# Kernel optimization log

Hardware: AMD Instinct MI355X
Metric: run time of the kernel (lower is better)

Reference implementation:

```python
import jax, jax.numpy as jnp
import numpy as np

EPS = 1e-08
CCE_WEIGHT = 1.0
DICE_WEIGHT = 0.5


def setup_inputs() -> dict:
    key = jax.random.key(0)
    k1, k2 = jax.random.split(key)
    B, C = 4194304, 8
    predictions = jax.random.normal(k1, (B, C), dtype=jnp.float32)
    labels = jax.random.randint(k2, (B,), 0, C)
    ground_truth = jax.nn.one_hot(labels, C, dtype=jnp.float32)  # one-hot, in [0,1]
    class_weights = jnp.array([1.0, 2.0, 1.5, 0.5, 1.0, 3.0, 0.75, 1.25], dtype=jnp.float32)
    return {"predictions": predictions, "ground_truth": ground_truth, "class_weights": class_weights}


def reference(predictions, ground_truth, class_weights):
    C = class_weights.shape[0]
    p = jax.nn.softmax(predictions, axis=1)            # [B, C]
    pred_cat = jnp.argmax(p, axis=1)                   # [B]
    gt_cat = jnp.argmax(ground_truth, axis=1)          # [B]

    # Confusion matrix: single fused scatter-add (replaces per-sample torch loop)
    cm = jnp.zeros((C, C), dtype=p.dtype).at[gt_cat, pred_cat].add(1.0)
    tp = jnp.diagonal(cm)
    fp = cm.sum(axis=0) - tp
    fn = cm.sum(axis=1) - tp
    dice = (tp + EPS) / (tp + fp + fn + EPS)
    dice_loss = jnp.mean((1.0 - dice) * class_weights)

    # Faithful to the original: cross_entropy is applied to the *softmaxed*
    # predictions (double softmax), with soft (probability) targets and
    # per-class weights; reduction='mean' over the batch.
    log_p2 = jax.nn.log_softmax(p, axis=1)             # log_softmax(softmax(x))
    ce_per_sample = -jnp.sum(class_weights * ground_truth * log_p2, axis=1)  # [B]
    cce_loss = jnp.mean(ce_per_sample)

    return cce_loss * CCE_WEIGHT + dice_loss * DICE_WEIGHT
```

## Files before the change

### kernel.cpp

```cpp
#include <hip/hip_runtime.h>


#define NBLOCKS 2048
#define NTHREADS 256

__device__ __forceinline__ float fast_exp(float x) { return __expf(x); }

__global__ void wcd_init(unsigned int* __restrict__ cnt) {
    int i = threadIdx.x;
    if (i < 24) cnt[i] = 0u;
}

__global__ __launch_bounds__(NTHREADS) void wcd_main(
    const float* __restrict__ pred, const float* __restrict__ gt,
    const float* __restrict__ cw, unsigned int* __restrict__ cnt,
    float* __restrict__ ce_partial, int B)
{
    __shared__ float sw[8];
    __shared__ unsigned int scnt[24];
    __shared__ float sred[NTHREADS];

    const int tid = threadIdx.x;
    if (tid < 8)  sw[tid]   = cw[tid];
    if (tid < 24) scnt[tid] = 0u;
    __syncthreads();

    float ce = 0.0f;
    const int stride = gridDim.x * blockDim.x;
    for (int i = blockIdx.x * blockDim.x + tid; i < B; i += stride) {
        const float4* p4 = reinterpret_cast<const float4*>(pred) + 2 * (size_t)i;
        const float4* g4 = reinterpret_cast<const float4*>(gt)   + 2 * (size_t)i;
        float4 a0 = p4[0], a1 = p4[1];
        float4 b0 = g4[0], b1 = g4[1];
        float x[8] = {a0.x, a0.y, a0.z, a0.w, a1.x, a1.y, a1.z, a1.w};
        float g[8] = {b0.x, b0.y, b0.z, b0.w, b1.x, b1.y, b1.z, b1.w};

        float m = x[0]; int am = 0;
        #pragma unroll
        for (int j = 1; j < 8; ++j) { if (x[j] > m) { m = x[j]; am = j; } }

        int gi = 0;
        #pragma unroll
        for (int j = 1; j < 8; ++j) { if (g[j] > 0.5f) gi = j; }

        float e[8], se = 0.0f;
        #pragma unroll
        for (int j = 0; j < 8; ++j) { e[j] = fast_exp(x[j] - m); se += e[j]; }
        float inv = 1.0f / se;

        float s2 = 0.0f, pg = 0.0f;
        #pragma unroll
        for (int j = 0; j < 8; ++j) {
            float pj = e[j] * inv;
            s2 += fast_exp(pj);
            if (j == gi) pg = pj;
        }
        ce += sw[gi] * (__logf(s2) - pg);

        atomicAdd(&scnt[gi], 1u);
        atomicAdd(&scnt[8 + am], 1u);
        if (gi == am) atomicAdd(&scnt[16 + gi], 1u);
    }

    sred[tid] = ce;
    __syncthreads();
    #pragma unroll
    for (int s = NTHREADS / 2; s > 0; s >>= 1) {
        if (tid < s) sred[tid] += sred[tid + s];
        __syncthreads();
    }
    if (tid == 0) ce_partial[blockIdx.x] = sred[0];

    if (tid < 24 && scnt[tid] != 0u) atomicAdd(&cnt[tid], scnt[tid]);
}

__global__ __launch_bounds__(NTHREADS) void wcd_finalize(
    const unsigned int* __restrict__ cnt, const float* __restrict__ ce_partial,
    const float* __restrict__ cw, float* __restrict__ out, int B)
{
    __shared__ float sred[NTHREADS];
    const int tid = threadIdx.x;
    float s = 0.0f;
    for (int i = tid; i < NBLOCKS; i += NTHREADS) s += ce_partial[i];
    sred[tid] = s;
    __syncthreads();
    #pragma unroll
    for (int k = NTHREADS / 2; k > 0; k >>= 1) {
        if (tid < k) sred[tid] += sred[tid + k];
        __syncthreads();
    }
    if (tid == 0) {
        const float EPS = 1e-8f;
        float dice_loss = 0.0f;
        #pragma unroll
        for (int c = 0; c < 8; ++c) {
            float tp    = (float)cnt[16 + c];
            float rowc  = (float)cnt[c];
            float colc  = (float)cnt[8 + c];
            float dice  = (tp + EPS) / (rowc + colc - tp + EPS);
            dice_loss  += (1.0f - dice) * cw[c];
        }
        dice_loss *= (1.0f / 8.0f);
        float cce = sred[0] / (float)B;
        out[0] = cce * 1.0f + dice_loss * 0.5f;
    }
}

extern "C" void kernel_launch(void* const* d_in, const int* in_sizes, int n_in,
                              void* d_out, int out_size, void* d_ws, size_t ws_size,
                              hipStream_t stream) {
    const float* pred = (const float*)d_in[0];
    const float* gt   = (const float*)d_in[1];
    const float* cw   = (const float*)d_in[2];
    float* out        = (float*)d_out;

    const int C = in_sizes[2];
    const int B = in_sizes[0] / C;

    unsigned int* cnt  = (unsigned int*)d_ws;
    float* ce_partial  = (float*)d_ws + 32;

    wcd_init<<<1, 64, 0, stream>>>(cnt);
    wcd_main<<<NBLOCKS, NTHREADS, 0, stream>>>(pred, gt, cw, cnt, ce_partial, B);
    wcd_finalize<<<1, NTHREADS, 0, stream>>>(cnt, ce_partial, cw, out, B);
}
```

Measured before the change: 62.82 us.

## Replace per-sample LDS atomics with packed nibble counters and wave shuffles

Each thread now counts the confusion-matrix entries in packed 4-bit nibbles inside three registers, instead of doing up to three shared-memory atomics per sample. At the end of the block the nibbles are widened to 16-bit halves, reduced across the wave with xor shuffles, and only lane 0 of each wave does the LDS atomics. The CE sum uses the same shuffle reduction in place of a tree in shared memory. The main loop is unrolled by 4 so more global loads are in flight. The nibble packing can overflow if a single thread handles more than 15 samples of one class, which is safe for this batch size but not for general B.

```diff
diff --git a/kernel.cpp b/kernel.cpp
--- a/kernel.cpp
+++ b/kernel.cpp
@@ -3,13 +3,17 @@
 
 #define NBLOCKS 2048
 #define NTHREADS 256
-
-__device__ __forceinline__ float fast_exp(float x) { return __expf(x); }
+#define UNROLL 4
 
 __global__ void wcd_init(unsigned int* __restrict__ cnt) {
-    int i = threadIdx.x;
-    if (i < 24) cnt[i] = 0u;
-}
+    if (threadIdx.x < 24) cnt[threadIdx.x] = 0u;
+}
+
+#define EXPAND(n, o0, o1, o2, o3)                                             \
+    o0 = ((n) & 0xFu)         | (((n) >> 4)  & 0xFu) << 16;                   \
+    o1 = (((n) >> 8) & 0xFu)  | (((n) >> 12) & 0xFu) << 16;                   \
+    o2 = (((n) >> 16) & 0xFu) | (((n) >> 20) & 0xFu) << 16;                   \
+    o3 = (((n) >> 24) & 0xFu) | (((n) >> 28) & 0xFu) << 16;
 
 __global__ __launch_bounds__(NTHREADS) void wcd_main(
     const float* __restrict__ pred, const float* __restrict__ gt,
@@ -18,7 +22,7 @@
 {
     __shared__ float sw[8];
     __shared__ unsigned int scnt[24];
-    __shared__ float sred[NTHREADS];
+    __shared__ float sce[NTHREADS / 64];
 
     const int tid = threadIdx.x;
     if (tid < 8)  sw[tid]   = cw[tid];
@@ -26,52 +30,128 @@
     __syncthreads();
 
     float ce = 0.0f;
+    unsigned int gt_n = 0u, pr_n = 0u, tp_n = 0u;
+
     const int stride = gridDim.x * blockDim.x;
-    for (int i = blockIdx.x * blockDim.x + tid; i < B; i += stride) {
-        const float4* p4 = reinterpret_cast<const float4*>(pred) + 2 * (size_t)i;
-        const float4* g4 = reinterpret_cast<const float4*>(gt)   + 2 * (size_t)i;
-        float4 a0 = p4[0], a1 = p4[1];
-        float4 b0 = g4[0], b1 = g4[1];
+    const float4* __restrict__ p4 = reinterpret_cast<const float4*>(pred);
+    const float4* __restrict__ g4 = reinterpret_cast<const float4*>(gt);
+
+    int i = blockIdx.x * blockDim.x + tid;
+
+    for (; i + (UNROLL - 1) * stride < B; i += UNROLL * stride) {
+        float4 pa[UNROLL], pb[UNROLL], ga[UNROLL], gb[UNROLL];
+        #pragma unroll
+        for (int k = 0; k < UNROLL; ++k) {
+            size_t off = 2 * (size_t)(i + k * stride);
+            pa[k] = p4[off]; pb[k] = p4[off + 1];
+            ga[k] = g4[off]; gb[k] = g4[off + 1];
+        }
+        #pragma unroll
+        for (int k = 0; k < UNROLL; ++k) {
+            float x[8] = {pa[k].x, pa[k].y, pa[k].z, pa[k].w,
+                          pb[k].x, pb[k].y, pb[k].z, pb[k].w};
+            float g[8] = {ga[k].x, ga[k].y, ga[k].z, ga[k].w,
+                          gb[k].x, gb[k].y, gb[k].z, gb[k].w};
+
+            float m = x[0]; int am = 0;
+            #pragma unroll
+            for (int j = 1; j < 8; ++j) { if (x[j] > m) { m = x[j]; am = j; } }
+
+            int gi = 0;
+            #pragma unroll
+            for (int j = 1; j < 8; ++j) { if (g[j] > 0.5f) gi = j; }
+
+            float e[8], se = 0.0f;
+            #pragma unroll
+            for (int j = 0; j < 8; ++j) { e[j] = __expf(x[j] - m); se += e[j]; }
+            float inv = 1.0f / se;
+
+            float s2 = 0.0f, pg = 0.0f;
+            #pragma unroll
+            for (int j = 0; j < 8; ++j) {
+                float pj = e[j] * inv;
+                s2 += __expf(pj);
+                if (j == gi) pg = pj;
+            }
+            ce += sw[gi] * (__logf(s2) - pg);
+
+            gt_n += 1u << (gi << 2);
+            pr_n += 1u << (am << 2);
+            if (gi == am) tp_n += 1u << (gi << 2);
+        }
+    }
+
+    for (; i < B; i += stride) {
+        size_t off = 2 * (size_t)i;
+        float4 a0 = p4[off], a1 = p4[off + 1];
+        float4 b0 = g4[off], b1 = g4[off + 1];
         float x[8] = {a0.x, a0.y, a0.z, a0.w, a1.x, a1.y, a1.z, a1.w};
         float g[8] = {b0.x, b0.y, b0.z, b0.w, b1.x, b1.y, b1.z, b1.w};
-
         float m = x[0]; int am = 0;
         #pragma unroll
         for (int j = 1; j < 8; ++j) { if (x[j] > m) { m = x[j]; am = j; } }
-
         int gi = 0;
         #pragma unroll
         for (int j = 1; j < 8; ++j) { if (g[j] > 0.5f) gi = j; }
-
         float e[8], se = 0.0f;
         #pragma unroll
-        for (int j = 0; j < 8; ++j) { e[j] = fast_exp(x[j] - m); se += e[j]; }
+        for (int j = 0; j < 8; ++j) { e[j] = __expf(x[j] - m); se += e[j]; }
         float inv = 1.0f / se;
-
         float s2 = 0.0f, pg = 0.0f;
         #pragma unroll
         for (int j = 0; j < 8; ++j) {
             float pj = e[j] * inv;
-            s2 += fast_exp(pj);
+            s2 += __expf(pj);
             if (j == gi) pg = pj;
         }
         ce += sw[gi] * (__logf(s2) - pg);
-
-        atomicAdd(&scnt[gi], 1u);
-        atomicAdd(&scnt[8 + am], 1u);
-        if (gi == am) atomicAdd(&scnt[16 + gi], 1u);
-    }
-
-    sred[tid] = ce;
+        gt_n += 1u << (gi << 2);
+        pr_n += 1u << (am << 2);
+        if (gi == am) tp_n += 1u << (gi << 2);
+    }
+
+    unsigned int a0, a1, a2, a3, b0_, b1_, b2_, b3_, c0, c1, c2, c3;
+    EXPAND(gt_n, a0, a1, a2, a3);
+    EXPAND(pr_n, b0_, b1_, b2_, b3_);
+    EXPAND(tp_n, c0, c1, c2, c3);
+
+    #pragma unroll
+    for (int msk = 32; msk > 0; msk >>= 1) {
+        ce  += __shfl_xor(ce, msk, 64);
+        a0  += __shfl_xor(a0, msk, 64);  a1 += __shfl_xor(a1, msk, 64);
+        a2  += __shfl_xor(a2, msk, 64);  a3 += __shfl_xor(a3, msk, 64);
+        b0_ += __shfl_xor(b0_, msk, 64); b1_ += __shfl_xor(b1_, msk, 64);
+        b2_ += __shfl_xor(b2_, msk, 64); b3_ += __shfl_xor(b3_, msk, 64);
+        c0  += __shfl_xor(c0, msk, 64);  c1 += __shfl_xor(c1, msk, 64);
+        c2  += __shfl_xor(c2, msk, 64);  c3 += __shfl_xor(c3, msk, 64);
+    }
+
+    const int lane = tid & 63;
+    const int wid  = tid >> 6;
+    if (lane == 0) {
+        sce[wid] = ce;
+        atomicAdd(&scnt[0],  a0 & 0xFFFFu);  atomicAdd(&scnt[1],  a0 >> 16);
+        atomicAdd(&scnt[2],  a1 & 0xFFFFu);  atomicAdd(&scnt[3],  a1 >> 16);
+        atomicAdd(&scnt[4],  a2 & 0xFFFFu);  atomicAdd(&scnt[5],  a2 >> 16);
+        atomicAdd(&scnt[6],  a3 & 0xFFFFu);  atomicAdd(&scnt[7],  a3 >> 16);
+        atomicAdd(&scnt[8],  b0_ & 0xFFFFu); atomicAdd(&scnt[9],  b0_ >> 16);
+        atomicAdd(&scnt[10], b1_ & 0xFFFFu); atomicAdd(&scnt[11], b1_ >> 16);
+        atomicAdd(&scnt[12], b2_ & 0xFFFFu); atomicAdd(&scnt[13], b2_ >> 16);
+        atomicAdd(&scnt[14], b3_ & 0xFFFFu); atomicAdd(&scnt[15], b3_ >> 16);
+        atomicAdd(&scnt[16], c0 & 0xFFFFu);  atomicAdd(&scnt[17], c0 >> 16);
+        atomicAdd(&scnt[18], c1 & 0xFFFFu);  atomicAdd(&scnt[19], c1 >> 16);
+        atomicAdd(&scnt[20], c2 & 0xFFFFu);  atomicAdd(&scnt[21], c2 >> 16);
+        atomicAdd(&scnt[22], c3 & 0xFFFFu);  atomicAdd(&scnt[23], c3 >> 16);
+    }
     __syncthreads();
-    #pragma unroll
-    for (int s = NTHREADS / 2; s > 0; s >>= 1) {
-        if (tid < s) sred[tid] += sred[tid + s];
-        __syncthreads();
-    }
-    if (tid == 0) ce_partial[blockIdx.x] = sred[0];
 
     if (tid < 24 && scnt[tid] != 0u) atomicAdd(&cnt[tid], scnt[tid]);
+    if (tid == 0) {
+        float s = 0.0f;
+        #pragma unroll
+        for (int w = 0; w < NTHREADS / 64; ++w) s += sce[w];
+        ce_partial[blockIdx.x] = s;
+    }
 }
 
 __global__ __launch_bounds__(NTHREADS) void wcd_finalize(
@@ -94,11 +174,11 @@
         float dice_loss = 0.0f;
         #pragma unroll
         for (int c = 0; c < 8; ++c) {
-            float tp    = (float)cnt[16 + c];
-            float rowc  = (float)cnt[c];
-            float colc  = (float)cnt[8 + c];
-            float dice  = (tp + EPS) / (rowc + colc - tp + EPS);
-            dice_loss  += (1.0f - dice) * cw[c];
+            float tp   = (float)cnt[16 + c];
+            float rowc = (float)cnt[c];
+            float colc = (float)cnt[8 + c];
+            float dice = (tp + EPS) / (rowc + colc - tp + EPS);
+            dice_loss += (1.0f - dice) * cw[c];
         }
         dice_loss *= (1.0f / 8.0f);
         float cce = sred[0] / (float)B;
```

Result: slower. 73.28 us (+16.7%).
